# Kernel tuning notes

Measured on AMD Instinct MI355X. Metric: run time of the kernel, lower is better.

The kernel has to match this reference:

```python
import jax, jax.numpy as jnp
import numpy as np

T, B, I, H = 2048, 32, 512, 512


def setup_inputs() -> dict:
    key = jax.random.key(0)
    ks = jax.random.split(key, 8)
    s = 1.0 / np.sqrt(H)
    return {
        "X": jax.random.normal(ks[0], (T, B, I), dtype=jnp.float32),
        "h": jax.random.normal(ks[1], (B, H), dtype=jnp.float32),
        "W_ih": jax.random.uniform(ks[2], (3 * H, I), jnp.float32, -s, s),
        "W_hh": jax.random.uniform(ks[3], (3 * H, H), jnp.float32, -s, s),
        "b_ih": jax.random.uniform(ks[4], (3 * H,), jnp.float32, -s, s),
        "b_hh": jax.random.uniform(ks[5], (3 * H,), jnp.float32, -s, s),
        "W_dense": jax.random.uniform(ks[6], (H, I), jnp.float32, -s, s),
        "b_dense": jax.random.uniform(ks[7], (H,), jnp.float32, -s, s),
    }


def reference(X, h, W_ih, W_hh, b_ih, b_hh, W_dense, b_dense):
    # Precompute input-side gate projections for all timesteps: [T, B, 3H]
    gi_all = jnp.einsum('tbi,gi->tbg', X, W_ih) + b_ih

    def step(h, gi):
        # hidden-side gates for this step: [B, 3H]
        gh = h @ W_hh.T + b_hh
        i_r, i_z, i_n = jnp.split(gi, 3, axis=-1)
        h_r, h_z, h_n = jnp.split(gh, 3, axis=-1)
        r = jax.nn.sigmoid(i_r + h_r)
        z = jax.nn.sigmoid(i_z + h_z)
        n = jnp.tanh(i_n + r * h_n)
        h_new = (1.0 - z) * n + z * h
        return h_new, h_new

    h_last, outputs = jax.lax.scan(step, h, gi_all)
    # AddNorm with dropout=0 (eval): dense(X) + outputs
    dense = jnp.einsum('tbi,hi->tbh', X, W_dense) + b_dense
    return outputs + dense, h_last
```

## Files before the change

kernel.cpp:

```cpp
#include <hip/hip_runtime.h>

#define TT   2048
#define NB   32
#define NI   512
#define NHID 512
#define NWG  32
#define KSL  16

typedef float    f32x4 __attribute__((ext_vector_type(4)));
typedef _Float16 f16x8 __attribute__((ext_vector_type(8)));

__device__ __align__(256) unsigned int g_flags[576];
__device__ __align__(256) _Float16    g_hb0[NB * NHID];
__device__ __align__(256) _Float16    g_hb1[NB * NHID];
__device__ __align__(256) _Float16    g_wfrag[NWG][4][16][64][8];

__device__ __forceinline__ f16x8 pack8(f32x4 a, f32x4 b) {
    f16x8 r;
    r[0] = (_Float16)a[0]; r[1] = (_Float16)a[1]; r[2] = (_Float16)a[2]; r[3] = (_Float16)a[3];
    r[4] = (_Float16)b[0]; r[5] = (_Float16)b[1]; r[6] = (_Float16)b[2]; r[7] = (_Float16)b[3];
    return r;
}

__device__ __forceinline__ unsigned int poll_load_nt(const unsigned int* p) {
    unsigned int v;
    asm volatile("global_load_dword %0, %1, off nt\n\ts_waitcnt vmcnt(0)"
                 : "=v"(v) : "v"(p) : "memory");
    return v;
}

extern "C" __global__ void init_flags_k() {
    for (int i = threadIdx.x; i < 576; i += 256) g_flags[i] = 0u;
}

extern "C" __global__ void pack_wfrag_k(const float* __restrict__ Wih,
                                        const float* __restrict__ Wd) {
    const int w    = blockIdx.x;
    const int tid  = threadIdx.x;
    const int lane = tid & 63;
    const int mat  = tid >> 6;
    const int r15  = lane & 15;
    const int g4   = lane >> 4;
    const float* src = (mat < 3) ? (Wih + (size_t)(mat * 512 + w * KSL + r15) * NI)
                                 : (Wd  + (size_t)(w * KSL + r15) * NI);
    #pragma unroll
    for (int kc = 0; kc < 16; ++kc) {
        const f32x4* p = (const f32x4*)(src + kc * 32 + g4 * 8);
        *(f16x8*)&g_wfrag[w][mat][kc][lane][0] = pack8(p[0], p[1]);
    }
}

extern "C" __global__ void __launch_bounds__(256, 1)
gru_persist(const float* __restrict__ X, const float* __restrict__ h0,
            const float* __restrict__ Wih, const float* __restrict__ Whh,
            const float* __restrict__ bih, const float* __restrict__ bhh,
            const float* __restrict__ Wd,  const float* __restrict__ bd,
            float* __restrict__ out)
{
    if (blockIdx.x & 7) return;
    const int w  = blockIdx.x >> 3;
    const int ks = w * KSL;

    __shared__ _Float16 fragWhh[3][16][64][8];
    __shared__ float    gi_lds[2][2][4][16][20];
    __shared__ float    bias_h[3][KSL];
    __shared__ float    bias_i[4][KSL];
    __shared__ unsigned int seq[16];
    __shared__ unsigned int fast_sh;
    volatile unsigned int* vseq = seq;

    const int tid  = threadIdx.x;
    const int lane = tid & 63;
    const int wv   = tid >> 6;
    const int half = wv & 1;
    const int isp  = wv >> 1;
    const int r15  = lane & 15;
    const int g4   = lane >> 4;

    if (tid < 16) seq[tid] = 0u;
    if (tid < KSL) {
        int k = ks + tid;
        bias_h[0][tid] = bhh[k];
        bias_h[1][tid] = bhh[512 + k];
        bias_h[2][tid] = bhh[1024 + k];
        bias_i[0][tid] = bih[k];
        bias_i[1][tid] = bih[512 + k];
        bias_i[2][tid] = bih[1024 + k];
        bias_i[3][tid] = bd[k];
    }
    if (wv < 3) {
        const float* src = Whh + (size_t)(wv * 512 + ks + r15) * NHID;
        #pragma unroll
        for (int kc = 0; kc < 16; ++kc) {
            const f32x4* p = (const f32x4*)(src + kc * 32 + g4 * 8);
            *(f16x8*)&fragWhh[wv][kc][lane][0] = pack8(p[0], p[1]);
        }
    }
    if (tid == 0) {
        unsigned int xcc;
        asm volatile("s_getreg_b32 %0, hwreg(HW_REG_XCC_ID, 0, 32)" : "=s"(xcc));
        unsigned int bit = 1u << (xcc & 7);
        unsigned int* mask  = g_flags + 512;
        unsigned int* count = g_flags + 513;
        unsigned int old = __hip_atomic_fetch_or(mask, bit, __ATOMIC_RELAXED,
                                                 __HIP_MEMORY_SCOPE_AGENT);
        asm volatile("" :: "v"(old));
        __hip_atomic_fetch_add(count, 1u, __ATOMIC_RELAXED, __HIP_MEMORY_SCOPE_AGENT);
        while (__hip_atomic_load(count, __ATOMIC_RELAXED,
                                 __HIP_MEMORY_SCOPE_AGENT) < NWG) { }
        unsigned int m = __hip_atomic_load(mask, __ATOMIC_RELAXED,
                                           __HIP_MEMORY_SCOPE_AGENT);
        fast_sh = ((m & (m - 1)) == 0) ? 1u : 0u;
    }
    __syncthreads();
    const bool fast = (fast_sh != 0);
    const int  bg   = half * 16 + r15;

    if (!isp) {
        __builtin_amdgcn_s_setprio(1);
        f32x4 hold = *(const f32x4*)(h0 + (size_t)bg * NHID + ks + g4 * 4);
        const f32x4 bhr = *(const f32x4*)&bias_h[0][g4 * 4];
        const f32x4 bhz = *(const f32x4*)&bias_h[1][g4 * 4];
        const f32x4 bhn = *(const f32x4*)&bias_h[2][g4 * 4];
        const f32x4 bir = *(const f32x4*)&bias_i[0][g4 * 4];
        const f32x4 biz = *(const f32x4*)&bias_i[1][g4 * 4];
        const f32x4 bin = *(const f32x4*)&bias_i[2][g4 * 4];
        const f32x4 bd4 = *(const f32x4*)&bias_i[3][g4 * 4];
        const float* h0row = h0 + (size_t)bg * NHID;

        #pragma unroll 1
        for (int t = 0; t < TT; ++t) {
            if (t > 0 && lane < NWG) {
                const unsigned int* fp = &g_flags[lane * 16 + half * 8];
                if (fast) { while (poll_load_nt(fp) < (unsigned)t) { } }
                else      { while (__hip_atomic_load(fp, __ATOMIC_RELAXED,
                                       __HIP_MEMORY_SCOPE_AGENT) < (unsigned)t) { } }
            }
            f16x8 Bf[16];
            if (t == 0) {
                #pragma unroll
                for (int kc = 0; kc < 16; ++kc) {
                    const f32x4* p = (const f32x4*)(h0row + kc * 32 + g4 * 8);
                    Bf[kc] = pack8(p[0], p[1]);
                }
            } else {
                const _Float16* hrow = ((t & 1) ? g_hb1 : g_hb0) + (size_t)bg * NHID;
                if (fast) {
                    #pragma unroll
                    for (int kc = 0; kc < 16; ++kc) {
                        const _Float16* p = hrow + kc * 32 + g4 * 8;
                        asm volatile("global_load_dwordx4 %0, %1, off nt"
                                     : "=v"(Bf[kc]) : "v"(p));
                    }
                } else {
                    #pragma unroll
                    for (int kc = 0; kc < 16; ++kc) {
                        const _Float16* p = hrow + kc * 32 + g4 * 8;
                        asm volatile("global_load_dwordx4 %0, %1, off sc0 sc1"
                                     : "=v"(Bf[kc]) : "v"(p));
                    }
                }
                asm volatile("s_waitcnt vmcnt(0)" ::: "memory");
                __builtin_amdgcn_sched_barrier(0);
            }
            f32x4 a0 = {0.f,0.f,0.f,0.f}, a1 = a0, a2 = a0;
            #pragma unroll
            for (int kc = 0; kc < 16; ++kc) {
                f16x8 w0 = *(const f16x8*)&fragWhh[0][kc][lane][0];
                f16x8 w1 = *(const f16x8*)&fragWhh[1][kc][lane][0];
                f16x8 w2 = *(const f16x8*)&fragWhh[2][kc][lane][0];
                a0 = __builtin_amdgcn_mfma_f32_16x16x32_f16(w0, Bf[kc], a0, 0, 0, 0);
                a1 = __builtin_amdgcn_mfma_f32_16x16x32_f16(w1, Bf[kc], a1, 0, 0, 0);
                a2 = __builtin_amdgcn_mfma_f32_16x16x32_f16(w2, Bf[kc], a2, 0, 0, 0);
            }
            while (vseq[half] < (unsigned)(t + 1)) { }
            const int par = t & 1;
            f32x4 gr = *(const f32x4*)&gi_lds[par][half][0][r15][g4 * 4];
            f32x4 gz = *(const f32x4*)&gi_lds[par][half][1][r15][g4 * 4];
            f32x4 gn = *(const f32x4*)&gi_lds[par][half][2][r15][g4 * 4];
            f32x4 gd = *(const f32x4*)&gi_lds[par][half][3][r15][g4 * 4];
            asm volatile("s_waitcnt lgkmcnt(0)" ::: "memory");
            if (lane == 0) vseq[2 + half] = (unsigned)(t + 1);
            f32x4 hn, o;
            #pragma unroll
            for (int i = 0; i < 4; ++i) {
                float rr = 1.f / (1.f + __expf(-((gr[i] + bir[i]) + (a0[i] + bhr[i]))));
                float zz = 1.f / (1.f + __expf(-((gz[i] + biz[i]) + (a1[i] + bhz[i]))));
                float aa = (gn[i] + bin[i]) + rr * (a2[i] + bhn[i]);
                float nn = 1.f - 2.f / (__expf(2.f * aa) + 1.f);
                hn[i] = (1.f - zz) * nn + zz * hold[i];
                o[i]  = hn[i] + gd[i] + bd4[i];
            }
            hold = hn;
            union { _Float16 h[4]; unsigned long long u; } cv;
            cv.h[0] = (_Float16)hn[0]; cv.h[1] = (_Float16)hn[1];
            cv.h[2] = (_Float16)hn[2]; cv.h[3] = (_Float16)hn[3];
            _Float16* hw = (((t + 1) & 1) ? g_hb1 : g_hb0) + (size_t)bg * NHID + ks + g4 * 4;
            if (fast) {
                *(unsigned long long*)hw = cv.u;
            } else {
                asm volatile("global_store_dwordx2 %0, %1, off sc0 sc1"
                             :: "v"(hw), "v"(cv.u) : "memory");
            }
            asm volatile("s_waitcnt vmcnt(0)" ::: "memory");
            if (lane == 0) {
                unsigned int* fp = &g_flags[w * 16 + half * 8];
                if (fast) *(volatile unsigned int*)fp = (unsigned)(t + 1);
                else __hip_atomic_store(fp, (unsigned)(t + 1), __ATOMIC_RELAXED,
                                        __HIP_MEMORY_SCOPE_AGENT);
            }
            *(f32x4*)(out + (size_t)t * (NB * NHID) + (size_t)bg * NHID + ks + g4 * 4) = o;
        }
        *(f32x4*)(out + (size_t)TT * (NB * NHID) + (size_t)bg * NHID + ks + g4 * 4) = hold;
    } else {
        __builtin_amdgcn_s_setprio(1);
        const float* Xrow = X + (size_t)bg * NI;

        #pragma unroll 1
        for (int tp = 0; tp < TT; ++tp) {
            while ((int)vseq[2 + half] < tp - 1) { }
            const float* xp = Xrow + (size_t)tp * (NB * NI);
            f16x8 Bf[16];
            #pragma unroll
            for (int kc = 0; kc < 16; ++kc) {
                const f32x4* p = (const f32x4*)(xp + kc * 32 + g4 * 8);
                Bf[kc] = pack8(p[0], p[1]);
            }
            f32x4 acc[4];
            #pragma unroll
            for (int q = 0; q < 4; ++q) acc[q] = (f32x4){0.f, 0.f, 0.f, 0.f};
            #pragma unroll
            for (int mat = 0; mat < 4; ++mat) {
                f16x8 wb[16];
                #pragma unroll
                for (int kc = 0; kc < 16; ++kc)
                    wb[kc] = *(const f16x8*)&g_wfrag[w][mat][kc][lane][0];
                #pragma unroll
                for (int kc = 0; kc < 16; ++kc)
                    acc[mat] = __builtin_amdgcn_mfma_f32_16x16x32_f16(wb[kc], Bf[kc], acc[mat], 0, 0, 0);
            }
            const int par = tp & 1;
            *(f32x4*)&gi_lds[par][half][0][r15][g4 * 4] = acc[0];
            *(f32x4*)&gi_lds[par][half][1][r15][g4 * 4] = acc[1];
            *(f32x4*)&gi_lds[par][half][2][r15][g4 * 4] = acc[2];
            *(f32x4*)&gi_lds[par][half][3][r15][g4 * 4] = acc[3];
            asm volatile("s_waitcnt lgkmcnt(0)" ::: "memory");
            if (lane == 0) vseq[half] = (unsigned)(tp + 1);
        }
    }
}

extern "C" void kernel_launch(void* const* d_in, const int* in_sizes, int n_in,
                              void* d_out, int out_size, void* d_ws, size_t ws_size,
                              hipStream_t stream) {
    const float* X   = (const float*)d_in[0];
    const float* h0  = (const float*)d_in[1];
    const float* Wih = (const float*)d_in[2];
    const float* Whh = (const float*)d_in[3];
    const float* bih = (const float*)d_in[4];
    const float* bhh = (const float*)d_in[5];
    const float* Wd  = (const float*)d_in[6];
    const float* bd  = (const float*)d_in[7];
    float* out = (float*)d_out;

    init_flags_k<<<dim3(1), dim3(256), 0, stream>>>();
    pack_wfrag_k<<<dim3(NWG), dim3(256), 0, stream>>>(Wih, Wd);

    gru_persist<<<dim3(256), dim3(256), 0, stream>>>(
        X, h0, Wih, Whh, bih, bhh, Wd, bd, out);
}
```

Before: 10.54 ms.

## Precompute input projections in a separate parallel GEMM kernel before recurrence

Moves the input-side and dense projections out of the persistent recurrent kernel into a standalone grid-wide GEMM kernel that stores gate inputs for every timestep in a global buffer. The recurrent kernel now runs only two waves per block and loads precomputed gates each step, issuing those loads before the flag wait. This is meant to take the producer waves and their LDS handshake off the serial critical path. The cost is a large global intermediate (about 512 MB) and an extra kernel pass before the recurrence starts.

After: 12.40 ms. 1.18x slower.

```diff
diff --git a/kernel.cpp b/kernel.cpp
--- a/kernel.cpp
+++ b/kernel.cpp
@@ -6,6 +6,7 @@
 #define NHID 512
 #define NWG  32
 #define KSL  16
+#define TCH  8
 
 typedef float    f32x4 __attribute__((ext_vector_type(4)));
 typedef _Float16 f16x8 __attribute__((ext_vector_type(8)));
@@ -13,7 +14,7 @@
 __device__ __align__(256) unsigned int g_flags[576];
 __device__ __align__(256) _Float16    g_hb0[NB * NHID];
 __device__ __align__(256) _Float16    g_hb1[NB * NHID];
-__device__ __align__(256) _Float16    g_wfrag[NWG][4][16][64][8];
+__device__ __align__(256) float       g_gi[TT][NWG][4][NB][16];
 
 __device__ __forceinline__ f16x8 pack8(f32x4 a, f32x4 b) {
     f16x8 r;
@@ -33,20 +34,59 @@
     for (int i = threadIdx.x; i < 576; i += 256) g_flags[i] = 0u;
 }
 
-extern "C" __global__ void pack_wfrag_k(const float* __restrict__ Wih,
-                                        const float* __restrict__ Wd) {
-    const int w    = blockIdx.x;
+extern "C" __global__ void __launch_bounds__(256, 1)
+gi_gemm(const float* __restrict__ X, const float* __restrict__ Wih,
+        const float* __restrict__ Wd)
+{
+    const int tc = blockIdx.x >> 5;
+    const int w  = blockIdx.x & 31;
+    __shared__ _Float16 wf[4][16][64][8];
+
     const int tid  = threadIdx.x;
     const int lane = tid & 63;
-    const int mat  = tid >> 6;
+    const int wv   = tid >> 6;
     const int r15  = lane & 15;
     const int g4   = lane >> 4;
-    const float* src = (mat < 3) ? (Wih + (size_t)(mat * 512 + w * KSL + r15) * NI)
-                                 : (Wd  + (size_t)(w * KSL + r15) * NI);
-    #pragma unroll
-    for (int kc = 0; kc < 16; ++kc) {
-        const f32x4* p = (const f32x4*)(src + kc * 32 + g4 * 8);
-        *(f16x8*)&g_wfrag[w][mat][kc][lane][0] = pack8(p[0], p[1]);
+
+    {
+        const float* src = (wv < 3) ? (Wih + (size_t)(wv * 512 + w * KSL + r15) * NI)
+                                    : (Wd  + (size_t)(w * KSL + r15) * NI);
+        #pragma unroll
+        for (int kc = 0; kc < 16; ++kc) {
+            const f32x4* p = (const f32x4*)(src + kc * 32 + g4 * 8);
+            *(f16x8*)&wf[wv][kc][lane][0] = pack8(p[0], p[1]);
+        }
+    }
+    __syncthreads();
+
+    const int half = wv & 1;
+    const int ts   = wv >> 1;
+    const int bg   = half * 16 + r15;
+
+    #pragma unroll 1
+    for (int tt = 0; tt < 4; ++tt) {
+        const int t = tc * TCH + ts * 4 + tt;
+        const float* xp = X + (size_t)t * (NB * NI) + (size_t)bg * NI;
+        f16x8 Bf[16];
+        #pragma unroll
+        for (int kc = 0; kc < 16; ++kc) {
+            const f32x4* p = (const f32x4*)(xp + kc * 32 + g4 * 8);
+            Bf[kc] = pack8(p[0], p[1]);
+        }
+        f32x4 acc[4];
+        #pragma unroll
+        for (int q = 0; q < 4; ++q) acc[q] = (f32x4){0.f, 0.f, 0.f, 0.f};
+        #pragma unroll
+        for (int kc = 0; kc < 16; ++kc) {
+            #pragma unroll
+            for (int mat = 0; mat < 4; ++mat) {
+                f16x8 wb = *(const f16x8*)&wf[mat][kc][lane][0];
+                acc[mat] = __builtin_amdgcn_mfma_f32_16x16x32_f16(wb, Bf[kc], acc[mat], 0, 0, 0);
+            }
+        }
+        #pragma unroll
+        for (int mat = 0; mat < 4; ++mat)
+            *(f32x4*)&g_gi[t][w][mat][bg][g4 * 4] = acc[mat];
     }
 }
 
@@ -62,22 +102,17 @@
     const int ks = w * KSL;
 
     __shared__ _Float16 fragWhh[3][16][64][8];
-    __shared__ float    gi_lds[2][2][4][16][20];
     __shared__ float    bias_h[3][KSL];
     __shared__ float    bias_i[4][KSL];
-    __shared__ unsigned int seq[16];
     __shared__ unsigned int fast_sh;
-    volatile unsigned int* vseq = seq;
 
     const int tid  = threadIdx.x;
     const int lane = tid & 63;
     const int wv   = tid >> 6;
     const int half = wv & 1;
-    const int isp  = wv >> 1;
     const int r15  = lane & 15;
     const int g4   = lane >> 4;
 
-    if (tid < 16) seq[tid] = 0u;
     if (tid < KSL) {
         int k = ks + tid;
         bias_h[0][tid] = bhh[k];
@@ -113,141 +148,103 @@
         fast_sh = ((m & (m - 1)) == 0) ? 1u : 0u;
     }
     __syncthreads();
+    if (wv >= 2) return;
+
     const bool fast = (fast_sh != 0);
     const int  bg   = half * 16 + r15;
 
-    if (!isp) {
-        __builtin_amdgcn_s_setprio(1);
-        f32x4 hold = *(const f32x4*)(h0 + (size_t)bg * NHID + ks + g4 * 4);
-        const f32x4 bhr = *(const f32x4*)&bias_h[0][g4 * 4];
-        const f32x4 bhz = *(const f32x4*)&bias_h[1][g4 * 4];
-        const f32x4 bhn = *(const f32x4*)&bias_h[2][g4 * 4];
-        const f32x4 bir = *(const f32x4*)&bias_i[0][g4 * 4];
-        const f32x4 biz = *(const f32x4*)&bias_i[1][g4 * 4];
-        const f32x4 bin = *(const f32x4*)&bias_i[2][g4 * 4];
-        const f32x4 bd4 = *(const f32x4*)&bias_i[3][g4 * 4];
-        const float* h0row = h0 + (size_t)bg * NHID;
-
-        #pragma unroll 1
-        for (int t = 0; t < TT; ++t) {
-            if (t > 0 && lane < NWG) {
-                const unsigned int* fp = &g_flags[lane * 16 + half * 8];
-                if (fast) { while (poll_load_nt(fp) < (unsigned)t) { } }
-                else      { while (__hip_atomic_load(fp, __ATOMIC_RELAXED,
-                                       __HIP_MEMORY_SCOPE_AGENT) < (unsigned)t) { } }
+    __builtin_amdgcn_s_setprio(1);
+    f32x4 hold = *(const f32x4*)(h0 + (size_t)bg * NHID + ks + g4 * 4);
+    const f32x4 bhr = *(const f32x4*)&bias_h[0][g4 * 4];
+    const f32x4 bhz = *(const f32x4*)&bias_h[1][g4 * 4];
+    const f32x4 bhn = *(const f32x4*)&bias_h[2][g4 * 4];
+    const f32x4 bir = *(const f32x4*)&bias_i[0][g4 * 4];
+    const f32x4 biz = *(const f32x4*)&bias_i[1][g4 * 4];
+    const f32x4 bin = *(const f32x4*)&bias_i[2][g4 * 4];
+    const f32x4 bd4 = *(const f32x4*)&bias_i[3][g4 * 4];
+    const float* h0row = h0 + (size_t)bg * NHID;
+
+    #pragma unroll 1
+    for (int t = 0; t < TT; ++t) {
+        const float* gp = &g_gi[t][w][0][bg][g4 * 4];
+        f32x4 gr = *(const f32x4*)(gp);
+        f32x4 gz = *(const f32x4*)(gp + 512);
+        f32x4 gn = *(const f32x4*)(gp + 1024);
+        f32x4 gd = *(const f32x4*)(gp + 1536);
+        if (t > 0 && lane < NWG) {
+            const unsigned int* fp = &g_flags[lane * 16 + half * 8];
+            if (fast) { while (poll_load_nt(fp) < (unsigned)t) { } }
+            else      { while (__hip_atomic_load(fp, __ATOMIC_RELAXED,
+                                   __HIP_MEMORY_SCOPE_AGENT) < (unsigned)t) { } }
+        }
+        f16x8 Bf[16];
+        if (t == 0) {
+            #pragma unroll
+            for (int kc = 0; kc < 16; ++kc) {
+                const f32x4* p = (const f32x4*)(h0row + kc * 32 + g4 * 8);
+                Bf[kc] = pack8(p[0], p[1]);
             }
-            f16x8 Bf[16];
-            if (t == 0) {
+        } else {
+            const _Float16* hrow = ((t & 1) ? g_hb1 : g_hb0) + (size_t)bg * NHID;
+            if (fast) {
                 #pragma unroll
                 for (int kc = 0; kc < 16; ++kc) {
-                    const f32x4* p = (const f32x4*)(h0row + kc * 32 + g4 * 8);
-                    Bf[kc] = pack8(p[0], p[1]);
+                    const _Float16* p = hrow + kc * 32 + g4 * 8;
+                    asm volatile("global_load_dwordx4 %0, %1, off nt"
+                                 : "=v"(Bf[kc]) : "v"(p));
                 }
             } else {
-                const _Float16* hrow = ((t & 1) ? g_hb1 : g_hb0) + (size_t)bg * NHID;
-                if (fast) {
-                    #pragma unroll
-                    for (int kc = 0; kc < 16; ++kc) {
-                        const _Float16* p = hrow + kc * 32 + g4 * 8;
-                        asm volatile("global_load_dwordx4 %0, %1, off nt"
-                                     : "=v"(Bf[kc]) : "v"(p));
-                    }
-                } else {
-                    #pragma unroll
-                    for (int kc = 0; kc < 16; ++kc) {
-                        const _Float16* p = hrow + kc * 32 + g4 * 8;
-                        asm volatile("global_load_dwordx4 %0, %1, off sc0 sc1"
-                                     : "=v"(Bf[kc]) : "v"(p));
-                    }
+                #pragma unroll
+                for (int kc = 0; kc < 16; ++kc) {
+                    const _Float16* p = hrow + kc * 32 + g4 * 8;
+                    asm volatile("global_load_dwordx4 %0, %1, off sc0 sc1"
+                                 : "=v"(Bf[kc]) : "v"(p));
                 }
-                asm volatile("s_waitcnt vmcnt(0)" ::: "memory");
-                __builtin_amdgcn_sched_barrier(0);
-            }
-            f32x4 a0 = {0.f,0.f,0.f,0.f}, a1 = a0, a2 = a0;
-            #pragma unroll
-            for (int kc = 0; kc < 16; ++kc) {
-                f16x8 w0 = *(const f16x8*)&fragWhh[0][kc][lane][0];
-                f16x8 w1 = *(const f16x8*)&fragWhh[1][kc][lane][0];
-                f16x8 w2 = *(const f16x8*)&fragWhh[2][kc][lane][0];
-                a0 = __builtin_amdgcn_mfma_f32_16x16x32_f16(w0, Bf[kc], a0, 0, 0, 0);
-                a1 = __builtin_amdgcn_mfma_f32_16x16x32_f16(w1, Bf[kc], a1, 0, 0, 0);
-                a2 = __builtin_amdgcn_mfma_f32_16x16x32_f16(w2, Bf[kc], a2, 0, 0, 0);
-            }
-            while (vseq[half] < (unsigned)(t + 1)) { }
-            const int par = t & 1;
-            f32x4 gr = *(const f32x4*)&gi_lds[par][half][0][r15][g4 * 4];
-            f32x4 gz = *(const f32x4*)&gi_lds[par][half][1][r15][g4 * 4];
-            f32x4 gn = *(const f32x4*)&gi_lds[par][half][2][r15][g4 * 4];
-            f32x4 gd = *(const f32x4*)&gi_lds[par][half][3][r15][g4 * 4];
-            asm volatile("s_waitcnt lgkmcnt(0)" ::: "memory");
-            if (lane == 0) vseq[2 + half] = (unsigned)(t + 1);
-            f32x4 hn, o;
-            #pragma unroll
-            for (int i = 0; i < 4; ++i) {
-                float rr = 1.f / (1.f + __expf(-((gr[i] + bir[i]) + (a0[i] + bhr[i]))));
-                float zz = 1.f / (1.f + __expf(-((gz[i] + biz[i]) + (a1[i] + bhz[i]))));
-                float aa = (gn[i] + bin[i]) + rr * (a2[i] + bhn[i]);
-                float nn = 1.f - 2.f / (__expf(2.f * aa) + 1.f);
-                hn[i] = (1.f - zz) * nn + zz * hold[i];
-                o[i]  = hn[i] + gd[i] + bd4[i];
-            }
-            hold = hn;
-            union { _Float16 h[4]; unsigned long long u; } cv;
-            cv.h[0] = (_Float16)hn[0]; cv.h[1] = (_Float16)hn[1];
-            cv.h[2] = (_Float16)hn[2]; cv.h[3] = (_Float16)hn[3];
-            _Float16* hw = (((t + 1) & 1) ? g_hb1 : g_hb0) + (size_t)bg * NHID + ks + g4 * 4;
-            if (fast) {
-                *(unsigned long long*)hw = cv.u;
-            } else {
-                asm volatile("global_store_dwordx2 %0, %1, off sc0 sc1"
-                             :: "v"(hw), "v"(cv.u) : "memory");
             }
             asm volatile("s_waitcnt vmcnt(0)" ::: "memory");
-            if (lane == 0) {
-                unsigned int* fp = &g_flags[w * 16 + half * 8];
-                if (fast) *(volatile unsigned int*)fp = (unsigned)(t + 1);
-                else __hip_atomic_store(fp, (unsigned)(t + 1), __ATOMIC_RELAXED,
-                                        __HIP_MEMORY_SCOPE_AGENT);
-            }
-            *(f32x4*)(out + (size_t)t * (NB * NHID) + (size_t)bg * NHID + ks + g4 * 4) = o;
-        }
-        *(f32x4*)(out + (size_t)TT * (NB * NHID) + (size_t)bg * NHID + ks + g4 * 4) = hold;
-    } else {
-        __builtin_amdgcn_s_setprio(1);
-        const float* Xrow = X + (size_t)bg * NI;
-
-        #pragma unroll 1
-        for (int tp = 0; tp < TT; ++tp) {
-            while ((int)vseq[2 + half] < tp - 1) { }
-            const float* xp = Xrow + (size_t)tp * (NB * NI);
-            f16x8 Bf[16];
-            #pragma unroll
-            for (int kc = 0; kc < 16; ++kc) {
-                const f32x4* p = (const f32x4*)(xp + kc * 32 + g4 * 8);
-                Bf[kc] = pack8(p[0], p[1]);
-            }
-            f32x4 acc[4];
-            #pragma unroll
-            for (int q = 0; q < 4; ++q) acc[q] = (f32x4){0.f, 0.f, 0.f, 0.f};
-            #pragma unroll
-            for (int mat = 0; mat < 4; ++mat) {
-                f16x8 wb[16];
-                #pragma unroll
-                for (int kc = 0; kc < 16; ++kc)
-                    wb[kc] = *(const f16x8*)&g_wfrag[w][mat][kc][lane][0];
-                #pragma unroll
-                for (int kc = 0; kc < 16; ++kc)
-                    acc[mat] = __builtin_amdgcn_mfma_f32_16x16x32_f16(wb[kc], Bf[kc], acc[mat], 0, 0, 0);
-            }
-            const int par = tp & 1;
-            *(f32x4*)&gi_lds[par][half][0][r15][g4 * 4] = acc[0];
-            *(f32x4*)&gi_lds[par][half][1][r15][g4 * 4] = acc[1];
-            *(f32x4*)&gi_lds[par][half][2][r15][g4 * 4] = acc[2];
-            *(f32x4*)&gi_lds[par][half][3][r15][g4 * 4] = acc[3];
-            asm volatile("s_waitcnt lgkmcnt(0)" ::: "memory");
-            if (lane == 0) vseq[half] = (unsigned)(tp + 1);
-        }
-    }
+            __builtin_amdgcn_sched_barrier(0);
+        }
+        f32x4 a0 = {0.f,0.f,0.f,0.f}, a1 = a0, a2 = a0;
+        #pragma unroll
+        for (int kc = 0; kc < 16; ++kc) {
+            f16x8 w0 = *(const f16x8*)&fragWhh[0][kc][lane][0];
+            f16x8 w1 = *(const f16x8*)&fragWhh[1][kc][lane][0];
+            f16x8 w2 = *(const f16x8*)&fragWhh[2][kc][lane][0];
+            a0 = __builtin_amdgcn_mfma_f32_16x16x32_f16(w0, Bf[kc], a0, 0, 0, 0);
+            a1 = __builtin_amdgcn_mfma_f32_16x16x32_f16(w1, Bf[kc], a1, 0, 0, 0);
+            a2 = __builtin_amdgcn_mfma_f32_16x16x32_f16(w2, Bf[kc], a2, 0, 0, 0);
+        }
+        f32x4 hn, o;
+        #pragma unroll
+        for (int i = 0; i < 4; ++i) {
+            float rr = 1.f / (1.f + __expf(-((gr[i] + bir[i]) + (a0[i] + bhr[i]))));
+            float zz = 1.f / (1.f + __expf(-((gz[i] + biz[i]) + (a1[i] + bhz[i]))));
+            float aa = (gn[i] + bin[i]) + rr * (a2[i] + bhn[i]);
+            float nn = 1.f - 2.f / (__expf(2.f * aa) + 1.f);
+            hn[i] = (1.f - zz) * nn + zz * hold[i];
+            o[i]  = hn[i] + gd[i] + bd4[i];
+        }
+        hold = hn;
+        union { _Float16 h[4]; unsigned long long u; } cv;
+        cv.h[0] = (_Float16)hn[0]; cv.h[1] = (_Float16)hn[1];
+        cv.h[2] = (_Float16)hn[2]; cv.h[3] = (_Float16)hn[3];
+        _Float16* hw = (((t + 1) & 1) ? g_hb1 : g_hb0) + (size_t)bg * NHID + ks + g4 * 4;
+        if (fast) {
+            *(unsigned long long*)hw = cv.u;
+        } else {
+            asm volatile("global_store_dwordx2 %0, %1, off sc0 sc1"
+                         :: "v"(hw), "v"(cv.u) : "memory");
+        }
+        asm volatile("s_waitcnt vmcnt(0)" ::: "memory");
+        if (lane == 0) {
+            unsigned int* fp = &g_flags[w * 16 + half * 8];
+            if (fast) *(volatile unsigned int*)fp = (unsigned)(t + 1);
+            else __hip_atomic_store(fp, (unsigned)(t + 1), __ATOMIC_RELAXED,
+                                    __HIP_MEMORY_SCOPE_AGENT);
+        }
+        *(f32x4*)(out + (size_t)t * (NB * NHID) + (size_t)bg * NHID + ks + g4 * 4) = o;
+    }
+    *(f32x4*)(out + (size_t)TT * (NB * NHID) + (size_t)bg * NHID + ks + g4 * 4) = hold;
 }
 
 extern "C" void kernel_launch(void* const* d_in, const int* in_sizes, int n_in,
@@ -264,7 +261,7 @@
     float* out = (float*)d_out;
 
     init_flags_k<<<dim3(1), dim3(256), 0, stream>>>();
-    pack_wfrag_k<<<dim3(NWG), dim3(256), 0, stream>>>(Wih, Wd);
+    gi_gemm<<<dim3((TT / TCH) * NWG), dim3(256), 0, stream>>>(X, Wih, Wd);
 
     gru_persist<<<dim3(256), dim3(256), 0, stream>>>(
         X, h0, Wih, Whh, bih, bhh, Wd, bd, out);
```
